# Optimization experiments

Hardware: AMD Instinct MI355X
Metric: run time of the kernel (lower is better)

## Reference

```python
import jax, jax.numpy as jnp
import numpy as np

N_NODES = 100000
N_EDGES = 800000
HID = 128
N_LAYERS = 3
N_GRAPHS = 64
LN_EPS = 1e-5


def setup_inputs() -> dict:
    key = jax.random.key(0)
    ks = jax.random.split(key, 12)
    s = 1.0 / np.sqrt(HID)  # xavier-ish scale
    return {
        "node_features": jax.random.normal(ks[0], (N_NODES, HID), jnp.float32),
        "edge_attr": jax.random.normal(ks[1], (N_EDGES, HID), jnp.float32),
        "in_proj_w": jax.random.normal(ks[2], (HID, HID), jnp.float32) * s,
        "in_proj_b": jnp.zeros((HID,), jnp.float32),
        "gcn_w": jax.random.normal(ks[3], (N_LAYERS, HID, HID), jnp.float32) * s,
        "gcn_ew": jax.random.normal(ks[4], (N_LAYERS, HID, HID), jnp.float32) * s,
        "gcn_b": jnp.zeros((N_LAYERS, HID), jnp.float32),
        "ln_scale": jnp.ones((N_LAYERS, HID), jnp.float32),
        "ln_bias": jnp.zeros((N_LAYERS, HID), jnp.float32),
        "out_proj_w": jax.random.normal(ks[5], (HID, HID), jnp.float32) * s,
        "out_proj_b": jnp.zeros((HID,), jnp.float32),
        "edge_index": jax.random.randint(ks[6], (2, N_EDGES), 0, N_NODES, jnp.int64),
        "batch": jnp.sort(jax.random.randint(ks[7], (N_NODES,), 0, N_GRAPHS, jnp.int64)),
    }


def _layer_norm(x, scale, bias):
    m = jnp.mean(x, axis=-1, keepdims=True)
    v = jnp.mean(jnp.square(x - m), axis=-1, keepdims=True)
    return (x - m) * jax.lax.rsqrt(v + LN_EPS) * scale + bias


def reference(node_features, edge_attr, in_proj_w, in_proj_b, gcn_w, gcn_ew,
              gcn_b, ln_scale, ln_bias, out_proj_w, out_proj_b,
              edge_index, batch):
    src, dst = edge_index[0], edge_index[1]
    x = node_features @ in_proj_w + in_proj_b  # [N, HID]
    for i in range(N_LAYERS):
        residual = x
        h = x @ gcn_w[i]                       # [N, HID]
        ew = edge_attr @ gcn_ew[i]             # [E, HID] edge gate
        msgs = h[src] * ew                     # [E, HID] gather + gate
        agg = jax.ops.segment_sum(msgs, dst, num_segments=N_NODES)  # scatter-add
        h = jax.nn.relu(agg + gcn_b[i])
        # dropout is identity in eval mode
        if i > 0:
            h = h + residual
        x = _layer_norm(h, ln_scale[i], ln_bias[i])
    x = x @ out_proj_w + out_proj_b            # [N, HID]
    # global mean pool per graph
    sums = jax.ops.segment_sum(x, batch, num_segments=N_GRAPHS)
    counts = jax.ops.segment_sum(jnp.ones((N_NODES,), x.dtype), batch,
                                 num_segments=N_GRAPHS)
    return sums / jnp.maximum(counts, 1.0)[:, None]  # [N_GRAPHS, HID]
```

## Files before the change

### kernel.cpp

```cpp
#include <hip/hip_runtime.h>

#define HID 128

typedef __attribute__((ext_vector_type(8))) short bf16x8;
typedef __attribute__((ext_vector_type(4))) float f32x4;
typedef __attribute__((ext_vector_type(4))) unsigned short u16x4;

__device__ __forceinline__ unsigned short f2bf(float f) {
  union { float f; unsigned u; } v; v.f = f;
  return (unsigned short)((v.u + 0x7FFFu + ((v.u >> 16) & 1u)) >> 16);
}
__device__ __forceinline__ float bf2f(unsigned short h) {
  union { unsigned u; float f; } v; v.u = ((unsigned)h) << 16; return v.f;
}


template<bool SRCF32, bool BIAS, bool OUTBF16>
__global__ __launch_bounds__(256, 3) void gemm_node_kernel(
    const void* __restrict__ Xv, const unsigned short* __restrict__ Wt,
    const float* __restrict__ bias, float* __restrict__ Yf,
    unsigned short* __restrict__ Yb, int nrows)
{
  const int tid  = threadIdx.x;
  const int lane = tid & 63;
  const int wave = tid >> 6;
  const int lr = lane & 15;
  const int lg = lane >> 4;
  const long row0 = (long)blockIdx.x * 128 + wave * 32;

  bf16x8 A[2][4];
  #pragma unroll
  for (int rt = 0; rt < 2; ++rt) {
    long R = row0 + rt * 16 + lr;
    if (R >= nrows) R = nrows - 1;
    if (SRCF32) {
      const float* xp = (const float*)Xv + R * HID;
      #pragma unroll
      for (int ks = 0; ks < 4; ++ks) {
        float4 lo = *(const float4*)(xp + ks * 32 + lg * 8);
        float4 hi = *(const float4*)(xp + ks * 32 + lg * 8 + 4);
        bf16x8 a;
        a[0] = (short)f2bf(lo.x); a[1] = (short)f2bf(lo.y);
        a[2] = (short)f2bf(lo.z); a[3] = (short)f2bf(lo.w);
        a[4] = (short)f2bf(hi.x); a[5] = (short)f2bf(hi.y);
        a[6] = (short)f2bf(hi.z); a[7] = (short)f2bf(hi.w);
        A[rt][ks] = a;
      }
    } else {
      const unsigned short* xp = (const unsigned short*)Xv + R * HID;
      #pragma unroll
      for (int ks = 0; ks < 4; ++ks)
        A[rt][ks] = *(const bf16x8*)(xp + ks * 32 + lg * 8);
    }
  }

  f32x4 acc[2][8];
  #pragma unroll
  for (int rt = 0; rt < 2; ++rt)
    #pragma unroll
    for (int ct = 0; ct < 8; ++ct)
      acc[rt][ct] = (f32x4){0.f, 0.f, 0.f, 0.f};

  #pragma unroll
  for (int ks = 0; ks < 4; ++ks) {
    bf16x8 Bf[8];
    #pragma unroll
    for (int ct = 0; ct < 8; ++ct)
      Bf[ct] = *(const bf16x8*)(Wt + (ct * 16 + lr) * HID + ks * 32 + lg * 8);
    #pragma unroll
    for (int rt = 0; rt < 2; ++rt)
      #pragma unroll
      for (int ct = 0; ct < 8; ++ct)
        acc[rt][ct] = __builtin_amdgcn_mfma_f32_16x16x32_bf16(
            A[rt][ks], Bf[ct], acc[rt][ct], 0, 0, 0);
  }

  #pragma unroll
  for (int rt = 0; rt < 2; ++rt) {
    #pragma unroll
    for (int r = 0; r < 4; ++r) {
      long e = row0 + rt * 16 + lg * 4 + r;
      if (e < nrows) {
        if (OUTBF16) {
          bf16x8 o;
          #pragma unroll
          for (int ct = 0; ct < 8; ++ct) {
            float v = acc[rt][ct][r];
            if (BIAS) v += bias[ct * 16 + lr];
            o[ct] = (short)f2bf(v);
          }
          *(bf16x8*)(Yb + e * HID + lr * 8) = o;
        } else {
          #pragma unroll
          for (int ct = 0; ct < 8; ++ct) {
            int col = ct * 16 + lr;
            float v = acc[rt][ct][r];
            if (BIAS) v += bias[col];
            Yf[e * HID + col] = v;
          }
        }
      }
    }
  }
}

__global__ __launch_bounds__(256, 3) void tri_edge_gemm_kernel(
    const float* __restrict__ EA, const int* __restrict__ perm,
    const unsigned short* __restrict__ Wt,
    unsigned short* __restrict__ msgs, int nE)
{
  const int tid  = threadIdx.x;
  const int lane = tid & 63;
  const int wave = tid >> 6;
  const int lr = lane & 15;
  const int lg = lane >> 4;
  const long row0 = (long)blockIdx.x * 128 + wave * 32;

  bf16x8 A[2][4];
  #pragma unroll
  for (int rt = 0; rt < 2; ++rt) {
    long R = row0 + rt * 16 + lr;
    const float* xp = EA + (long)perm[R] * HID;
    #pragma unroll
    for (int ks = 0; ks < 4; ++ks) {
      float4 lo = *(const float4*)(xp + ks * 32 + lg * 8);
      float4 hi = *(const float4*)(xp + ks * 32 + lg * 8 + 4);
      bf16x8 a;
      a[0] = (short)f2bf(lo.x); a[1] = (short)f2bf(lo.y);
      a[2] = (short)f2bf(lo.z); a[3] = (short)f2bf(lo.w);
      a[4] = (short)f2bf(hi.x); a[5] = (short)f2bf(hi.y);
      a[6] = (short)f2bf(hi.z); a[7] = (short)f2bf(hi.w);
      A[rt][ks] = a;
    }
  }

  #pragma unroll 1
  for (int w = 0; w < 3; ++w) {
    const unsigned short* Wp = Wt + (size_t)w * 16384;
    unsigned short* Mp = msgs + (size_t)w * nE * HID;

    f32x4 acc[2][8];
    #pragma unroll
    for (int rt = 0; rt < 2; ++rt)
      #pragma unroll
      for (int ct = 0; ct < 8; ++ct)
        acc[rt][ct] = (f32x4){0.f, 0.f, 0.f, 0.f};

    #pragma unroll
    for (int ks = 0; ks < 4; ++ks) {
      bf16x8 Bf[8];
      #pragma unroll
      for (int ct = 0; ct < 8; ++ct)
        Bf[ct] = *(const bf16x8*)(Wp + (ct * 16 + lr) * HID + ks * 32 + lg * 8);
      #pragma unroll
      for (int rt = 0; rt < 2; ++rt)
        #pragma unroll
        for (int ct = 0; ct < 8; ++ct)
          acc[rt][ct] = __builtin_amdgcn_mfma_f32_16x16x32_bf16(
              A[rt][ks], Bf[ct], acc[rt][ct], 0, 0, 0);
    }

    #pragma unroll
    for (int rt = 0; rt < 2; ++rt) {
      #pragma unroll
      for (int r = 0; r < 4; ++r) {
        long e = row0 + rt * 16 + lg * 4 + r;
        bf16x8 o;
        #pragma unroll
        for (int ct = 0; ct < 8; ++ct) o[ct] = (short)f2bf(acc[rt][ct][r]);
        *(bf16x8*)(Mp + e * HID + lr * 8) = o;
      }
    }
  }
}

__global__ __launch_bounds__(128) void seg_reduce_kernel(
    const unsigned short* __restrict__ msgs, const unsigned short* __restrict__ Hb,
    const int* __restrict__ ssrc, const int* __restrict__ segend,
    float* __restrict__ agg)
{
  const int t = threadIdx.x;
  const int dbase = blockIdx.x * 8;
  int p = (dbase == 0) ? 0 : segend[dbase - 1];
  #pragma unroll 1
  for (int j = 0; j < 8; ++j) {
    const int end = segend[dbase + j];
    float a0 = 0.f, a1 = 0.f;
    int q = p;
    for (; q + 1 < end; q += 2) {
      int s0 = ssrc[q];
      int s1 = ssrc[q + 1];
      float m0 = bf2f(msgs[(long)q * HID + t]);
      float h0 = bf2f(Hb[(long)s0 * HID + t]);
      float m1 = bf2f(msgs[(long)(q + 1) * HID + t]);
      float h1 = bf2f(Hb[(long)s1 * HID + t]);
      a0 += m0 * h0;
      a1 += m1 * h1;
    }
    if (q < end) {
      int s = ssrc[q];
      a0 += bf2f(msgs[(long)q * HID + t]) * bf2f(Hb[(long)s * HID + t]);
    }
    agg[(long)(dbase + j) * HID + t] = a0 + a1;
    p = end;
  }
}

__global__ __launch_bounds__(256, 3) void gemm_edge_fb_kernel(
    const float* __restrict__ EA, const int* __restrict__ perm,
    const unsigned short* __restrict__ Wt, const unsigned short* __restrict__ Hb,
    const int* __restrict__ ssrc, const int* __restrict__ sdst,
    float* __restrict__ agg, int nE)
{
  const int tid  = threadIdx.x;
  const int lane = tid & 63;
  const int wave = tid >> 6;
  const int lr = lane & 15;
  const int lg = lane >> 4;
  const long row0 = (long)blockIdx.x * 128 + wave * 32;

  bf16x8 A[2][4];
  #pragma unroll
  for (int rt = 0; rt < 2; ++rt) {
    long R = row0 + rt * 16 + lr;
    const float* xp = EA + (long)perm[R] * HID;
    #pragma unroll
    for (int ks = 0; ks < 4; ++ks) {
      float4 lo = *(const float4*)(xp + ks * 32 + lg * 8);
      float4 hi = *(const float4*)(xp + ks * 32 + lg * 8 + 4);
      bf16x8 a;
      a[0] = (short)f2bf(lo.x); a[1] = (short)f2bf(lo.y);
      a[2] = (short)f2bf(lo.z); a[3] = (short)f2bf(lo.w);
      a[4] = (short)f2bf(hi.x); a[5] = (short)f2bf(hi.y);
      a[6] = (short)f2bf(hi.z); a[7] = (short)f2bf(hi.w);
      A[rt][ks] = a;
    }
  }

  f32x4 acc[2][8];
  #pragma unroll
  for (int rt = 0; rt < 2; ++rt)
    #pragma unroll
    for (int ct = 0; ct < 8; ++ct)
      acc[rt][ct] = (f32x4){0.f, 0.f, 0.f, 0.f};

  #pragma unroll
  for (int ks = 0; ks < 4; ++ks) {
    bf16x8 Bf[8];
    #pragma unroll
    for (int ct = 0; ct < 8; ++ct)
      Bf[ct] = *(const bf16x8*)(Wt + (ct * 16 + lr) * HID + ks * 32 + lg * 8);
    #pragma unroll
    for (int rt = 0; rt < 2; ++rt)
      #pragma unroll
      for (int ct = 0; ct < 8; ++ct)
        acc[rt][ct] = __builtin_amdgcn_mfma_f32_16x16x32_bf16(
            A[rt][ks], Bf[ct], acc[rt][ct], 0, 0, 0);
  }

  #pragma unroll
  for (int rt = 0; rt < 2; ++rt) {
    const long base = row0 + rt * 16 + lg * 4;
    int4 sv = *(const int4*)(ssrc + base);
    int4 dv = *(const int4*)(sdst + base);
    bf16x8 hv0 = *(const bf16x8*)(Hb + (long)sv.x * HID + lr * 8);
    bf16x8 hv1 = *(const bf16x8*)(Hb + (long)sv.y * HID + lr * 8);
    bf16x8 hv2 = *(const bf16x8*)(Hb + (long)sv.z * HID + lr * 8);
    bf16x8 hv3 = *(const bf16x8*)(Hb + (long)sv.w * HID + lr * 8);

    float am[8];
    #pragma unroll
    for (int ct = 0; ct < 8; ++ct)
      am[ct] = acc[rt][ct][0] * bf2f((unsigned short)hv0[ct]);
    int dprev = dv.x;
    {
      bool same = (dv.y == dprev);
      if (!same) {
        float* ap = agg + (long)dprev * HID + lr;
        #pragma unroll
        for (int ct = 0; ct < 8; ++ct) atomicAdd(ap + ct * 16, am[ct]);
      }
      #pragma unroll
      for (int ct = 0; ct < 8; ++ct) {
        float m = acc[rt][ct][1] * bf2f((unsigned short)hv1[ct]);
        am[ct] = same ? am[ct] + m : m;
      }
      dprev = dv.y;
    }
    {
      bool same = (dv.z == dprev);
      if (!same) {
        float* ap = agg + (long)dprev * HID + lr;
        #pragma unroll
        for (int ct = 0; ct < 8; ++ct) atomicAdd(ap + ct * 16, am[ct]);
      }
      #pragma unroll
      for (int ct = 0; ct < 8; ++ct) {
        float m = acc[rt][ct][2] * bf2f((unsigned short)hv2[ct]);
        am[ct] = same ? am[ct] + m : m;
      }
      dprev = dv.z;
    }
    {
      bool same = (dv.w == dprev);
      if (!same) {
        float* ap = agg + (long)dprev * HID + lr;
        #pragma unroll
        for (int ct = 0; ct < 8; ++ct) atomicAdd(ap + ct * 16, am[ct]);
      }
      #pragma unroll
      for (int ct = 0; ct < 8; ++ct) {
        float m = acc[rt][ct][3] * bf2f((unsigned short)hv3[ct]);
        am[ct] = same ? am[ct] + m : m;
      }
      dprev = dv.w;
    }
    float* ap = agg + (long)dprev * HID + lr;
    #pragma unroll
    for (int ct = 0; ct < 8; ++ct) atomicAdd(ap + ct * 16, am[ct]);
  }
}

__global__ void hist_kernel(const int* __restrict__ dst, int nE,
                            int* __restrict__ hist)
{
  int i = blockIdx.x * 256 + threadIdx.x;
  if (i < nE) atomicAdd(&hist[dst[i]], 1);
}

__global__ __launch_bounds__(256) void scan1_kernel(
    const int* __restrict__ hist, int n, int* __restrict__ partial)
{
  __shared__ int buf[256];
  int t = threadIdx.x;
  int i = blockIdx.x * 256 + t;
  buf[t] = (i < n) ? hist[i] : 0;
  __syncthreads();
  #pragma unroll
  for (int off = 128; off >= 1; off >>= 1) {
    if (t < off) buf[t] += buf[t + off];
    __syncthreads();
  }
  if (t == 0) partial[blockIdx.x] = buf[0];
}

__global__ __launch_bounds__(512) void scan2_kernel(int* __restrict__ partial,
                                                    int nb)
{
  __shared__ int buf[512];
  int t = threadIdx.x;
  buf[t] = (t < nb) ? partial[t] : 0;
  __syncthreads();
  for (int off = 1; off < 512; off <<= 1) {
    int v = (t >= off) ? buf[t - off] : 0;
    __syncthreads();
    buf[t] += v;
    __syncthreads();
  }
  if (t < nb) partial[t] = (t == 0) ? 0 : buf[t - 1];
}

__global__ __launch_bounds__(256) void scan3_kernel(
    const int* __restrict__ hist, const int* __restrict__ partial,
    int* __restrict__ cursor, int n)
{
  __shared__ int buf[256];
  int t = threadIdx.x;
  int i = blockIdx.x * 256 + t;
  int v = (i < n) ? hist[i] : 0;
  buf[t] = v;
  __syncthreads();
  for (int off = 1; off < 256; off <<= 1) {
    int w = (t >= off) ? buf[t - off] : 0;
    __syncthreads();
    buf[t] += w;
    __syncthreads();
  }
  if (i < n) cursor[i] = partial[blockIdx.x] + buf[t] - v;
}

__global__ void scatter_kernel(const int* __restrict__ src,
                               const int* __restrict__ dst, int nE,
                               int* __restrict__ cursor,
                               int* __restrict__ perm,
                               int* __restrict__ ssrc, int* __restrict__ sdst)
{
  int e = blockIdx.x * 256 + threadIdx.x;
  if (e < nE) {
    int d = dst[e];
    int pos = atomicAdd(&cursor[d], 1);
    perm[pos] = e;
    ssrc[pos] = src[e];
    sdst[pos] = d;
  }
}

__global__ __launch_bounds__(256) void prep_w_kernel(
    const float* __restrict__ ipw, const float* __restrict__ gw,
    const float* __restrict__ gew, const float* __restrict__ opw,
    unsigned short* __restrict__ wt)
{
  int idx = blockIdx.x * 1024 + threadIdx.x * 4;
  #pragma unroll
  for (int t = 0; t < 4; ++t) {
    int i = idx + t;
    int m = i >> 14, r = i & 16383;
    int n = r >> 7, k = r & 127;
    const float* srcm;
    bool kperm;
    if (m == 0)      { srcm = ipw; kperm = false; }
    else if (m <= 3) { srcm = gw  + (size_t)(m - 1) * 16384; kperm = true; }
    else if (m <= 6) { srcm = gew + (size_t)(m - 4) * 16384; kperm = false; }
    else             { srcm = opw; kperm = true; }
    int kk = kperm ? ((k & 7) * 16 + (k >> 3)) : k;
    wt[i] = f2bf(srcm[kk * HID + n]);
  }
}

__global__ void prep_params_kernel(const float* __restrict__ gb,
                                   const float* __restrict__ lns,
                                   const float* __restrict__ lnb,
                                   float* __restrict__ bp,
                                   float* __restrict__ lsp,
                                   float* __restrict__ lbp)
{
  int idx = threadIdx.x + blockIdx.x * 128;
  if (idx < 384) {
    int i = idx >> 7, p = idx & 127;
    int c = (p & 7) * 16 + (p >> 3);
    bp[idx]  = gb[i * 128 + c];
    lsp[idx] = lns[i * 128 + c];
    lbp[idx] = lnb[i * 128 + c];
  }
}

__global__ __launch_bounds__(256) void ln_perm_kernel(
    const float* __restrict__ agg, const float* __restrict__ b,
    const float* res, const float* __restrict__ lnS,
    const float* __restrict__ lnB, float* xf, unsigned short* __restrict__ xb,
    int n)
{
  const int wave = threadIdx.x >> 6;
  const int lane = threadIdx.x & 63;
  const long node = (long)blockIdx.x * 4 + wave;
  if (node >= n) return;

  float2 v = *(const float2*)&agg[node * HID + lane * 2];
  float2 bb = *(const float2*)&b[lane * 2];
  v.x += bb.x; v.y += bb.y;
  v.x = fmaxf(v.x, 0.f); v.y = fmaxf(v.y, 0.f);
  if (res != nullptr) {
    float2 rr = *(const float2*)&res[node * HID + lane * 2];
    v.x += rr.x; v.y += rr.y;
  }
  float s = v.x + v.y;
  #pragma unroll
  for (int off = 32; off >= 1; off >>= 1) s += __shfl_xor(s, off);
  float mean = s * (1.f / 128.f);
  float dx = v.x - mean, dy = v.y - mean;
  float q = dx * dx + dy * dy;
  #pragma unroll
  for (int off = 32; off >= 1; off >>= 1) q += __shfl_xor(q, off);
  float rstd = rsqrtf(q * (1.f / 128.f) + 1e-5f);
  float2 sc = *(const float2*)&lnS[lane * 2];
  float2 sb = *(const float2*)&lnB[lane * 2];
  float ox = dx * rstd * sc.x + sb.x;
  float oy = dy * rstd * sc.y + sb.y;
  *(float2*)&xf[node * HID + lane * 2] = make_float2(ox, oy);
  unsigned pk = (unsigned)f2bf(ox) | ((unsigned)f2bf(oy) << 16);
  *(unsigned*)&xb[node * HID + lane * 2] = pk;
}

__global__ __launch_bounds__(256) void ln_nat_kernel(
    const float* __restrict__ agg, const float* __restrict__ b,
    const float* res, const float* __restrict__ lnS,
    const float* __restrict__ lnB, float* xf, unsigned short* __restrict__ xb,
    int n)
{
  const int wave = threadIdx.x >> 6;
  const int lane = threadIdx.x & 63;
  const long node = (long)blockIdx.x * 4 + wave;
  if (node >= n) return;

  float2 v = *(const float2*)&agg[node * HID + lane * 2];
  float2 bb = *(const float2*)&b[lane * 2];
  v.x += bb.x; v.y += bb.y;
  v.x = fmaxf(v.x, 0.f); v.y = fmaxf(v.y, 0.f);
  if (res != nullptr) {
    float2 rr = *(const float2*)&res[node * HID + lane * 2];
    v.x += rr.x; v.y += rr.y;
  }
  float s = v.x + v.y;
  #pragma unroll
  for (int off = 32; off >= 1; off >>= 1) s += __shfl_xor(s, off);
  float mean = s * (1.f / 128.f);
  float dx = v.x - mean, dy = v.y - mean;
  float q = dx * dx + dy * dy;
  #pragma unroll
  for (int off = 32; off >= 1; off >>= 1) q += __shfl_xor(q, off);
  float rstd = rsqrtf(q * (1.f / 128.f) + 1e-5f);
  float2 sc = *(const float2*)&lnS[lane * 2];
  float2 sb = *(const float2*)&lnB[lane * 2];
  float ox = dx * rstd * sc.x + sb.x;
  float oy = dy * rstd * sc.y + sb.y;
  *(float2*)&xf[node * HID + lane * 2] = make_float2(ox, oy);
  int c0 = lane * 2, c1 = lane * 2 + 1;
  xb[node * HID + ((c0 & 15) * 8 + (c0 >> 4))] = f2bf(ox);
  xb[node * HID + ((c1 & 15) * 8 + (c1 >> 4))] = f2bf(oy);
}

__global__ void graph_count_kernel(const int* __restrict__ batch, int n,
                                   int nG, int* __restrict__ counts)
{
  int g = threadIdx.x;
  if (g >= nG) return;
  int lo0 = 0, hi0 = n;
  while (lo0 < hi0) { int mid = (lo0 + hi0) >> 1; if (batch[mid] < g) lo0 = mid + 1; else hi0 = mid; }
  int lo1 = lo0, hi1 = n;
  while (lo1 < hi1) { int mid = (lo1 + hi1) >> 1; if (batch[mid] < g + 1) lo1 = mid + 1; else hi1 = mid; }
  counts[g] = lo1 - lo0;
}

__global__ __launch_bounds__(128) void pool_kernel(
    const float* __restrict__ X, const int* __restrict__ batch, int n,
    float* __restrict__ sums)
{
  const int col = threadIdx.x;
  long n0 = (long)blockIdx.x * 64;
  long n1 = n0 + 64; if (n1 > n) n1 = n;
  if (n0 >= n) return;
  float s = 0.f;
  int g = batch[n0];
  for (long i = n0; i < n1; ++i) {
    int gi = batch[i];
    if (gi != g) {
      atomicAdd(&sums[g * HID + col], s);
      s = 0.f;
      g = gi;
    }
    s += X[i * HID + col];
  }
  atomicAdd(&sums[g * HID + col], s);
}

__global__ void finalize_kernel(const float* __restrict__ sums,
                                const int* __restrict__ counts,
                                float* __restrict__ out, int total)
{
  int i = blockIdx.x * 256 + threadIdx.x;
  if (i < total) {
    int g = i >> 7;
    float c = (float)counts[g];
    out[i] = sums[i] / fmaxf(c, 1.f);
  }
}

extern "C" void kernel_launch(void* const* d_in, const int* in_sizes, int n_in,
                              void* d_out, int out_size, void* d_ws, size_t ws_size,
                              hipStream_t stream)
{
  const float* nf    = (const float*)d_in[0];
  const float* ea    = (const float*)d_in[1];
  const float* ipw   = (const float*)d_in[2];
  const float* ipb   = (const float*)d_in[3];
  const float* gw    = (const float*)d_in[4];
  const float* gew   = (const float*)d_in[5];
  const float* gb    = (const float*)d_in[6];
  const float* lns   = (const float*)d_in[7];
  const float* lnb   = (const float*)d_in[8];
  const float* opw   = (const float*)d_in[9];
  const float* opb   = (const float*)d_in[10];
  const int*   ei    = (const int*)d_in[11];
  const int*   batch = (const int*)d_in[12];
  float* out = (float*)d_out;

  const int N = 100000;
  const int E = 800000;
  const int G = 64;
  const int* srcI = ei;
  const int* dstI = ei + E;

  char* ws = (char*)d_ws;
  const size_t nodeF = (size_t)N * HID * sizeof(float);
  const size_t nodeB = (size_t)N * HID * sizeof(unsigned short);
  size_t off = 0;
  float*          xf   = (float*)(ws + off); off += nodeF;
  float*          agg  = (float*)(ws + off); off += nodeF;
  unsigned short* xb   = (unsigned short*)(ws + off); off += nodeB;
  unsigned short* hb   = (unsigned short*)(ws + off); off += nodeB;
  unsigned short* wt   = (unsigned short*)(ws + off); off += 8 * 16384 * 2;
  float*          bp   = (float*)(ws + off); off += 384 * 4;
  float*          lsp  = (float*)(ws + off); off += 384 * 4;
  float*          lbp  = (float*)(ws + off); off += 384 * 4;
  int*            perm = (int*)(ws + off); off += (size_t)E * 4;
  int*            ssrc = (int*)(ws + off); off += (size_t)E * 4;
  int*            sdst = (int*)(ws + off); off += (size_t)E * 4;
  int*            hist = (int*)(ws + off); off += (size_t)N * 4;
  int*            curs = (int*)(ws + off); off += (size_t)N * 4;
  int*            part = (int*)(ws + off); off += 512 * 4;
  float*          sums = (float*)(ws + off); off += (size_t)G * HID * 4;
  int*            cnts = (int*)(ws + off); off += G * 4;
  unsigned short* msgs = (unsigned short*)(ws + off);
  off += 3 * (size_t)E * HID * sizeof(unsigned short);
  const bool hoisted = (ws_size >= off);

  dim3 blk(256);
  const int nBlkN = (N + 127) / 128;
  const int nBlkE = E / 128;
  const int nBins = (N + 255) / 256;

  prep_w_kernel<<<128, blk, 0, stream>>>(ipw, gw, gew, opw, wt);
  prep_params_kernel<<<3, dim3(128), 0, stream>>>(gb, lns, lnb, bp, lsp, lbp);

  hipMemsetAsync(hist, 0, (size_t)N * 4, stream);
  hist_kernel<<<(E + 255) / 256, blk, 0, stream>>>(dstI, E, hist);
  scan1_kernel<<<nBins, blk, 0, stream>>>(hist, N, part);
  scan2_kernel<<<1, dim3(512), 0, stream>>>(part, nBins);
  scan3_kernel<<<nBins, blk, 0, stream>>>(hist, part, curs, N);
  scatter_kernel<<<(E + 255) / 256, blk, 0, stream>>>(srcI, dstI, E, curs,
                                                      perm, ssrc, sdst);

  if (hoisted) {
    tri_edge_gemm_kernel<<<nBlkE, blk, 0, stream>>>(
        ea, perm, wt + (size_t)4 * 16384, msgs, E);
  }

  gemm_node_kernel<true, true, true><<<nBlkN, blk, 0, stream>>>(
      nf, wt, ipb, nullptr, xb, N);

  for (int i = 0; i < 3; ++i) {
    gemm_node_kernel<false, false, true><<<nBlkN, blk, 0, stream>>>(
        xb, wt + (size_t)(1 + i) * 16384, nullptr, nullptr, hb, N);
    if (hoisted) {
      seg_reduce_kernel<<<N / 8, dim3(128), 0, stream>>>(
          msgs + (size_t)i * E * HID, hb, ssrc, curs, agg);
      ln_perm_kernel<<<(N + 3) / 4, blk, 0, stream>>>(
          agg, bp + i * HID, (i > 0) ? xf : nullptr, lsp + i * HID,
          lbp + i * HID, xf, xb, N);
    } else {
      hipMemsetAsync(agg, 0, nodeF, stream);
      gemm_edge_fb_kernel<<<nBlkE, blk, 0, stream>>>(
          ea, perm, wt + (size_t)(4 + i) * 16384, hb, ssrc, sdst, agg, E);
      ln_nat_kernel<<<(N + 3) / 4, blk, 0, stream>>>(
          agg, gb + i * HID, (i > 0) ? xf : nullptr, lns + i * HID,
          lnb + i * HID, xf, xb, N);
    }
  }

  gemm_node_kernel<false, true, false><<<nBlkN, blk, 0, stream>>>(
      xb, wt + (size_t)7 * 16384, opb, agg, nullptr, N);

  graph_count_kernel<<<1, dim3(64), 0, stream>>>(batch, N, G, cnts);
  hipMemsetAsync(sums, 0, (size_t)G * HID * 4, stream);
  pool_kernel<<<(N + 63) / 64, dim3(128), 0, stream>>>(agg, batch, N, sums);
  finalize_kernel<<<(G * HID + 255) / 256, blk, 0, stream>>>(
      sums, cnts, out, G * HID);
}
```

Baseline: 1.067 ms.

## Fuse layer norm into segment reduce and stage edge gather via shared memory

```diff
diff --git a/kernel.cpp b/kernel.cpp
--- a/kernel.cpp
+++ b/kernel.cpp
@@ -109,29 +109,37 @@
     const unsigned short* __restrict__ Wt,
     unsigned short* __restrict__ msgs, int nE)
 {
+  __shared__ unsigned short sA[128 * 144];
+  __shared__ int sPerm[128];
   const int tid  = threadIdx.x;
   const int lane = tid & 63;
   const int wave = tid >> 6;
   const int lr = lane & 15;
   const int lg = lane >> 4;
-  const long row0 = (long)blockIdx.x * 128 + wave * 32;
+  const long row0 = (long)blockIdx.x * 128;
+
+  if (tid < 128) sPerm[tid] = perm[row0 + tid];
+  __syncthreads();
+
+  #pragma unroll
+  for (int i = 0; i < 16; ++i) {
+    int idx = tid + i * 256;
+    int row = idx >> 5, part = idx & 31;
+    const float* xp = EA + (long)sPerm[row] * HID + part * 4;
+    float4 v = *(const float4*)xp;
+    u16x4 o;
+    o[0] = f2bf(v.x); o[1] = f2bf(v.y); o[2] = f2bf(v.z); o[3] = f2bf(v.w);
+    *(u16x4*)(sA + row * 144 + part * 4) = o;
+  }
+  __syncthreads();
 
   bf16x8 A[2][4];
   #pragma unroll
   for (int rt = 0; rt < 2; ++rt) {
-    long R = row0 + rt * 16 + lr;
-    const float* xp = EA + (long)perm[R] * HID;
-    #pragma unroll
-    for (int ks = 0; ks < 4; ++ks) {
-      float4 lo = *(const float4*)(xp + ks * 32 + lg * 8);
-      float4 hi = *(const float4*)(xp + ks * 32 + lg * 8 + 4);
-      bf16x8 a;
-      a[0] = (short)f2bf(lo.x); a[1] = (short)f2bf(lo.y);
-      a[2] = (short)f2bf(lo.z); a[3] = (short)f2bf(lo.w);
-      a[4] = (short)f2bf(hi.x); a[5] = (short)f2bf(hi.y);
-      a[6] = (short)f2bf(hi.z); a[7] = (short)f2bf(hi.w);
-      A[rt][ks] = a;
-    }
+    int rl = wave * 32 + rt * 16 + lr;
+    #pragma unroll
+    for (int ks = 0; ks < 4; ++ks)
+      A[rt][ks] = *(const bf16x8*)(sA + rl * 144 + ks * 32 + lg * 8);
   }
 
   #pragma unroll 1
@@ -164,7 +172,7 @@
     for (int rt = 0; rt < 2; ++rt) {
       #pragma unroll
       for (int r = 0; r < 4; ++r) {
-        long e = row0 + rt * 16 + lg * 4 + r;
+        long e = row0 + wave * 32 + rt * 16 + lg * 4 + r;
         bf16x8 o;
         #pragma unroll
         for (int ct = 0; ct < 8; ++ct) o[ct] = (short)f2bf(acc[rt][ct][r]);
@@ -174,17 +182,28 @@
   }
 }
 
-__global__ __launch_bounds__(128) void seg_reduce_kernel(
+__global__ __launch_bounds__(128) void seg_ln_kernel(
     const unsigned short* __restrict__ msgs, const unsigned short* __restrict__ Hb,
     const int* __restrict__ ssrc, const int* __restrict__ segend,
-    float* __restrict__ agg)
-{
+    const float* __restrict__ b, const float* __restrict__ lnS,
+    const float* __restrict__ lnB, const float* res,
+    float* __restrict__ xf, unsigned short* __restrict__ xb)
+{
+  __shared__ float2 red[2][8];
   const int t = threadIdx.x;
+  const int w = t >> 6;
+  const int lane = t & 63;
   const int dbase = blockIdx.x * 8;
+
+  const float bb = b[t];
+  const float sc = lnS[t];
+  const float sb = lnB[t];
+
   int p = (dbase == 0) ? 0 : segend[dbase - 1];
   #pragma unroll 1
   for (int j = 0; j < 8; ++j) {
-    const int end = segend[dbase + j];
+    const long node = dbase + j;
+    const int end = segend[node];
     float a0 = 0.f, a1 = 0.f;
     int q = p;
     for (; q + 1 < end; q += 2) {
@@ -201,8 +220,27 @@
       int s = ssrc[q];
       a0 += bf2f(msgs[(long)q * HID + t]) * bf2f(Hb[(long)s * HID + t]);
     }
-    agg[(long)(dbase + j) * HID + t] = a0 + a1;
     p = end;
+
+    float v = fmaxf(a0 + a1 + bb, 0.f);
+    if (res != nullptr) v += res[node * HID + t];
+
+    float s = v, qq = v * v;
+    #pragma unroll
+    for (int off = 32; off >= 1; off >>= 1) {
+      s  += __shfl_xor(s, off);
+      qq += __shfl_xor(qq, off);
+    }
+    if (lane == 0) red[w][j] = make_float2(s, qq);
+    __syncthreads();
+    float2 t0 = red[0][j], t1 = red[1][j];
+    float S = t0.x + t1.x, Q = t0.y + t1.y;
+    float mean = S * (1.f / 128.f);
+    float var = Q * (1.f / 128.f) - mean * mean;
+    float rstd = rsqrtf(var + 1e-5f);
+    float o = (v - mean) * rstd * sc + sb;
+    xf[node * HID + t] = o;
+    xb[node * HID + t] = f2bf(o);
   }
 }
 
@@ -432,43 +470,6 @@
     lsp[idx] = lns[i * 128 + c];
     lbp[idx] = lnb[i * 128 + c];
   }
-}
-
-__global__ __launch_bounds__(256) void ln_perm_kernel(
-    const float* __restrict__ agg, const float* __restrict__ b,
-    const float* res, const float* __restrict__ lnS,
-    const float* __restrict__ lnB, float* xf, unsigned short* __restrict__ xb,
-    int n)
-{
-  const int wave = threadIdx.x >> 6;
-  const int lane = threadIdx.x & 63;
-  const long node = (long)blockIdx.x * 4 + wave;
-  if (node >= n) return;
-
-  float2 v = *(const float2*)&agg[node * HID + lane * 2];
-  float2 bb = *(const float2*)&b[lane * 2];
-  v.x += bb.x; v.y += bb.y;
-  v.x = fmaxf(v.x, 0.f); v.y = fmaxf(v.y, 0.f);
-  if (res != nullptr) {
-    float2 rr = *(const float2*)&res[node * HID + lane * 2];
-    v.x += rr.x; v.y += rr.y;
-  }
-  float s = v.x + v.y;
-  #pragma unroll
-  for (int off = 32; off >= 1; off >>= 1) s += __shfl_xor(s, off);
-  float mean = s * (1.f / 128.f);
-  float dx = v.x - mean, dy = v.y - mean;
-  float q = dx * dx + dy * dy;
-  #pragma unroll
-  for (int off = 32; off >= 1; off >>= 1) q += __shfl_xor(q, off);
-  float rstd = rsqrtf(q * (1.f / 128.f) + 1e-5f);
-  float2 sc = *(const float2*)&lnS[lane * 2];
-  float2 sb = *(const float2*)&lnB[lane * 2];
-  float ox = dx * rstd * sc.x + sb.x;
-  float oy = dy * rstd * sc.y + sb.y;
-  *(float2*)&xf[node * HID + lane * 2] = make_float2(ox, oy);
-  unsigned pk = (unsigned)f2bf(ox) | ((unsigned)f2bf(oy) << 16);
-  *(unsigned*)&xb[node * HID + lane * 2] = pk;
 }
 
 __global__ __launch_bounds__(256) void ln_nat_kernel(
@@ -632,11 +633,10 @@
     gemm_node_kernel<false, false, true><<<nBlkN, blk, 0, stream>>>(
         xb, wt + (size_t)(1 + i) * 16384, nullptr, nullptr, hb, N);
     if (hoisted) {
-      seg_reduce_kernel<<<N / 8, dim3(128), 0, stream>>>(
-          msgs + (size_t)i * E * HID, hb, ssrc, curs, agg);
-      ln_perm_kernel<<<(N + 3) / 4, blk, 0, stream>>>(
-          agg, bp + i * HID, (i > 0) ? xf : nullptr, lsp + i * HID,
-          lbp + i * HID, xf, xb, N);
+      seg_ln_kernel<<<N / 8, dim3(128), 0, stream>>>(
+          msgs + (size_t)i * E * HID, hb, ssrc, curs,
+          bp + i * HID, lsp + i * HID, lbp + i * HID,
+          (i > 0) ? xf : nullptr, xf, xb);
     } else {
       hipMemsetAsync(agg, 0, nodeF, stream);
       gemm_edge_fb_kernel<<<nBlkE, blk, 0, stream>>>(
```

Measured after the change: 1.025 ms. -3.9%, faster.
